# Kernel optimization log

Measured on AMD Instinct MI355X. Metric: run time of the kernel, lower is better.

Reference implementation:

```python
import jax, jax.numpy as jnp
import numpy as np

B, C, H, W = 4, 256, 128, 128
K = 3
BN = max(16, C // 4)  # 64
PAD = K // 2
EPS = 1e-5


def conv2d(x, w, b=None, pad=0):
    out = jax.lax.conv_general_dilated(
        x, w, (1, 1), [(pad, pad), (pad, pad)],
        dimension_numbers=("NCHW", "OIHW", "NCHW"))
    if b is not None:
        out = out + b[None, :, None, None]
    return out


def deform_conv2d(z, offset, mask, w, b):
    # torchvision modulated deform conv v2: offset [B,2*K*K,H,W] interleaved (dy,dx),
    # mask [B,K*K,H,W], kernel positions row-major, stride 1, pad PAD.
    Bz, Cb, Hz, Wz = z.shape
    K2 = K * K
    off = offset.reshape(Bz, K2, 2, Hz, Wz)
    ky, kx = jnp.meshgrid(jnp.arange(K), jnp.arange(K), indexing="ij")
    # sampling positions py/px: [B, K2, H, W]
    py = off[:, :, 0] + jnp.arange(Hz)[None, None, :, None] + (ky.reshape(K2) - PAD)[None, :, None, None]
    px = off[:, :, 1] + jnp.arange(Wz)[None, None, None, :] + (kx.reshape(K2) - PAD)[None, :, None, None]
    y0 = jnp.floor(py)
    x0 = jnp.floor(px)
    wy1 = py - y0  # frac weights
    wx1 = px - x0
    z_flat = z.reshape(Bz, Cb, Hz * Wz)

    def gather(yy, xx, wgt):
        valid = (yy >= 0) & (yy < Hz) & (xx >= 0) & (xx < Wz)
        yc = jnp.clip(yy, 0, Hz - 1).astype(jnp.int32)
        xc = jnp.clip(xx, 0, Wz - 1).astype(jnp.int32)
        idx = (yc * Wz + xc).reshape(Bz, K2 * Hz * Wz)
        g = jnp.take_along_axis(z_flat, idx[:, None, :], axis=2)  # [B, Cb, K2*H*W]
        g = g.reshape(Bz, Cb, K2, Hz, Wz)
        return g * (wgt * valid.astype(z.dtype))[:, None]

    val = (gather(y0, x0, (1 - wy1) * (1 - wx1))
           + gather(y0, x0 + 1, (1 - wy1) * wx1)
           + gather(y0 + 1, x0, wy1 * (1 - wx1))
           + gather(y0 + 1, x0 + 1, wy1 * wx1))
    val = val * mask[:, None]  # modulate: [B, Cb, K2, H, W]
    out = jnp.einsum("bckhw,ock->bohw", val, w.reshape(w.shape[0], Cb, K2))
    return out + b[None, :, None, None]


def setup_inputs() -> dict:
    key = jax.random.key(0)
    ks = jax.random.split(key, 11)
    s = 0.05
    return {
        "x": jax.random.normal(ks[0], (B, C, H, W), jnp.float32),
        "down_w": jax.random.normal(ks[1], (BN, C, 1, 1), jnp.float32) * s,
        "off_w": jax.random.normal(ks[2], (2 * K * K, BN, 3, 3), jnp.float32) * s,
        "off_b": jax.random.normal(ks[3], (2 * K * K,), jnp.float32) * s,
        "mask_w": jax.random.normal(ks[4], (K * K, BN, 3, 3), jnp.float32) * s,
        "mask_b": jax.random.normal(ks[5], (K * K,), jnp.float32) * s,
        "def_w": jax.random.normal(ks[6], (BN, BN, K, K), jnp.float32) * s,
        "def_b": jax.random.normal(ks[7], (BN,), jnp.float32) * s,
        "up_w": jax.random.normal(ks[8], (C, BN, 1, 1), jnp.float32) * s,
        "gamma": jnp.ones((C,), jnp.float32),
        "beta": jnp.zeros((C,), jnp.float32),
    }


def reference(x, down_w, off_w, off_b, mask_w, mask_b, def_w, def_b, up_w, gamma, beta):
    z = conv2d(x, down_w)                               # 1x1 down: [B, BN, H, W]
    offset = conv2d(z, off_w, off_b, pad=1)             # [B, 18, H, W]
    mask = jax.nn.sigmoid(conv2d(z, mask_w, mask_b, pad=1))  # [B, 9, H, W]
    z = deform_conv2d(z, offset, mask, def_w, def_b)    # [B, BN, H, W]
    z = conv2d(z, up_w)                                 # 1x1 up: [B, C, H, W]
    y = x + z
    # BatchNorm2d in training mode: batch statistics over (B, H, W), biased var
    mean = jnp.mean(y, axis=(0, 2, 3), keepdims=True)
    var = jnp.var(y, axis=(0, 2, 3), keepdims=True)
    yh = (y - mean) * jax.lax.rsqrt(var + EPS)
    yh = yh * gamma[None, :, None, None] + beta[None, :, None, None]
    return yh * jax.nn.sigmoid(yh)  # SiLU
```

## Files before the change

kernel.cpp:

```cpp
#include <hip/hip_runtime.h>
#include <hip/hip_bf16.h>


typedef __attribute__((ext_vector_type(8))) short bf16x8;
typedef __attribute__((ext_vector_type(4))) short bf16x4;
typedef __attribute__((ext_vector_type(4))) float f32x4;

#define HW   16384
#define CC   256
#define BNC  64

#define WS_STATS   0
#define WS_SS      131072
#define WS_FD      135168
#define WS_FOM     167936
#define WS_FDEF    204800
#define WS_FUP     278528
#define WS_ZBF     311296
#define WS_OM      8699904
#define WS_Z2      15777792

__device__ __forceinline__ short f2b(float f) {
    unsigned u = __float_as_uint(f);
    unsigned r = (u + 0x7FFFu + ((u >> 16) & 1u)) >> 16;
    return (short)r;
}
__device__ __forceinline__ float b2f(short s) {
    return __uint_as_float(((unsigned)(unsigned short)s) << 16);
}

__global__ void k_prep(const float* __restrict__ down_w, const float* __restrict__ off_w,
                       const float* __restrict__ mask_w, const float* __restrict__ def_w,
                       const float* __restrict__ up_w, char* __restrict__ ws) {
    int g = blockIdx.x * 256 + threadIdx.x;
    int row = g >> 6, lane = g & 63;
    if (row >= 172) return;
    int l15 = lane & 15, q = lane >> 4;
    short vals[8];
    short* dst;
    if (row < 32) {
        int nt = row >> 3, kk = row & 7;
        int n = nt * 16 + l15;
        for (int j = 0; j < 8; ++j) {
            int c = kk * 32 + q * 8 + j;
            vals[j] = f2b(down_w[n * 256 + c]);
        }
        dst = (short*)(ws + WS_FD) + row * 512 + lane * 8;
    } else if (row < 68) {
        int r = row - 32; int nt = r / 18, kk = r % 18;
        int n = nt * 16 + l15;
        for (int j = 0; j < 8; ++j) {
            int kap = kk * 32 + q * 8 + j; int k = kap >> 6, c = kap & 63;
            float v = 0.f;
            if (n < 18)      v = off_w[(n * 64 + c) * 9 + k];
            else if (n < 27) v = mask_w[((n - 18) * 64 + c) * 9 + k];
            vals[j] = f2b(v);
        }
        dst = (short*)(ws + WS_FOM) + r * 512 + lane * 8;
    } else if (row < 140) {
        int r = row - 68; int nt = r / 18, kk = r % 18;
        int n = nt * 16 + l15;
        int u = kk * 4 + q, k = u >> 3;
        for (int j = 0; j < 8; ++j) {
            int c = (u & 7) * 8 + j;
            vals[j] = f2b(def_w[(n * 64 + c) * 9 + k]);
        }
        dst = (short*)(ws + WS_FDEF) + r * 512 + lane * 8;
    } else {
        int r = row - 140; int nt = r >> 1, kk = r & 1;
        int o = nt * 16 + l15;
        for (int j = 0; j < 8; ++j) {
            int c = kk * 32 + q * 8 + j;
            vals[j] = f2b(up_w[o * 64 + c]);
        }
        dst = (short*)(ws + WS_FUP) + r * 512 + lane * 8;
    }
    for (int j = 0; j < 8; ++j) dst[j] = vals[j];
}

__global__ __launch_bounds__(256) void k_down(const float* __restrict__ x,
                                              const short* __restrict__ wfd,
                                              short* __restrict__ zbf) {
    __shared__ __align__(16) short xl[64 * 264];
    int blk = blockIdx.x;
    int b = blk >> 8;
    int hw0 = (blk & 255) * 64;
    int t = threadIdx.x;
    const float* xb = x + (size_t)b * CC * HW + hw0;
    int px = t & 63, w = t >> 6;
    for (int h = 0; h < 8; ++h) {
        int c0 = h * 32 + w * 8;
        bf16x8 pk;
        #pragma unroll
        for (int j = 0; j < 8; ++j)
            pk[j] = f2b(xb[(size_t)(c0 + j) * HW + px]);
        *(bf16x8*)(&xl[px * 264 + c0]) = pk;
    }
    __syncthreads();
    int lane = t & 63, wv = t >> 6;
    int l15 = lane & 15, q = lane >> 4;
    bf16x8 A[8];
    const short* xrow = &xl[(wv * 16 + l15) * 264];
    for (int kk = 0; kk < 8; ++kk)
        A[kk] = *(const bf16x8*)(xrow + kk * 32 + q * 8);
    const bf16x8* Bp = (const bf16x8*)wfd;
    size_t obase = ((size_t)b * HW + hw0 + wv * 16) * 64;
    for (int nt = 0; nt < 4; ++nt) {
        f32x4 acc = {0.f, 0.f, 0.f, 0.f};
        for (int kk = 0; kk < 8; ++kk) {
            bf16x8 Bf = Bp[(nt * 8 + kk) * 64 + lane];
            acc = __builtin_amdgcn_mfma_f32_16x16x32_bf16(A[kk], Bf, acc, 0, 0, 0);
        }
        int n = nt * 16 + l15;
        for (int r = 0; r < 4; ++r) {
            int prow = q * 4 + r;
            zbf[obase + (size_t)prow * 64 + n] = f2b(acc[r]);
        }
    }
}

__global__ __launch_bounds__(256) void k_offmask(const short* __restrict__ zbf,
                                                 const short* __restrict__ wfom,
                                                 const float* __restrict__ off_b,
                                                 const float* __restrict__ mask_b,
                                                 float* __restrict__ om) {
    int blk = blockIdx.x;
    int b = blk >> 8;
    int hw0 = (blk & 255) * 64;
    int y = hw0 >> 7, x0 = hw0 & 127;
    int t = threadIdx.x, lane = t & 63, wv = t >> 6;
    int l15 = lane & 15, q = lane >> 4;
    int xx0 = x0 + wv * 16 + l15;
    const short* zb = zbf + (size_t)b * HW * 64;
    f32x4 acc0 = {0, 0, 0, 0}, acc1 = {0, 0, 0, 0};
    const bf16x8* Bp = (const bf16x8*)wfom;
    for (int kk = 0; kk < 18; ++kk) {
        int k = kk >> 1;
        int yy = y + (k / 3) - 1;
        int xx = xx0 + (k % 3) - 1;
        int c0 = (kk & 1) * 32 + q * 8;
        bf16x8 A = {0, 0, 0, 0, 0, 0, 0, 0};
        if (yy >= 0 && yy < 128 && xx >= 0 && xx < 128)
            A = *(const bf16x8*)(zb + ((size_t)(yy * 128 + xx)) * 64 + c0);
        bf16x8 B0 = Bp[kk * 64 + lane];
        bf16x8 B1 = Bp[(18 + kk) * 64 + lane];
        acc0 = __builtin_amdgcn_mfma_f32_16x16x32_bf16(A, B0, acc0, 0, 0, 0);
        acc1 = __builtin_amdgcn_mfma_f32_16x16x32_bf16(A, B1, acc1, 0, 0, 0);
    }
    float* omb = om + ((size_t)b * HW + hw0 + wv * 16) * 27;
    for (int half = 0; half < 2; ++half) {
        f32x4 acc = half ? acc1 : acc0;
        int n = half * 16 + l15;
        if (n < 27) {
            for (int r = 0; r < 4; ++r) {
                int prow = q * 4 + r;
                float v = acc[r];
                if (n < 18) v += off_b[n];
                else { v += mask_b[n - 18]; v = 1.f / (1.f + __expf(-v)); }
                omb[prow * 27 + n] = v;
            }
        }
    }
}

__global__ __launch_bounds__(256) void k_deform(const short* __restrict__ zbf,
                                                const float* __restrict__ om,
                                                const short* __restrict__ wfdef,
                                                const float* __restrict__ def_b,
                                                short* __restrict__ z2) {
    __shared__ int4   pAi4[144];
    __shared__ float4 pAw4[144];
    __shared__ __align__(16) short valA[18 * 64 * 8];
    int blk = blockIdx.x;
    int b = blk >> 10;
    int hw0 = (blk & 1023) * 16;
    int y = hw0 >> 7, x0 = hw0 & 127;
    int t = threadIdx.x;
    if (t < 144) {
        int px = t / 9, k = t % 9;
        const float* p = om + ((size_t)b * HW + hw0 + px) * 27;
        float dy = p[2 * k], dx = p[2 * k + 1], m = p[18 + k];
        float py  = (float)y + (float)(k / 3 - 1) + dy;
        float pxf = (float)(x0 + px) + (float)(k % 3 - 1) + dx;
        float fy = floorf(py), fx = floorf(pxf);
        int iy = (int)fy, ix = (int)fx;
        float wy = py - fy, wx = pxf - fx;
        float ww[4] = { (1.f - wy) * (1.f - wx) * m, (1.f - wy) * wx * m,
                        wy * (1.f - wx) * m,          wy * wx * m };
        int ys[2] = {iy, iy + 1}, xs[2] = {ix, ix + 1};
        int   ri[4]; float rw[4];
        for (int ci = 0; ci < 4; ++ci) {
            int cy = ys[ci >> 1], cx = xs[ci & 1];
            bool v = (cy >= 0 && cy < 128 && cx >= 0 && cx < 128);
            ri[ci] = v ? (cy * 128 + cx) * 64 : 0;
            rw[ci] = v ? ww[ci] : 0.f;
        }
        pAi4[t] = make_int4(ri[0], ri[1], ri[2], ri[3]);
        pAw4[t] = make_float4(rw[0], rw[1], rw[2], rw[3]);
    }
    __syncthreads();
    const unsigned short* zb = (const unsigned short*)zbf + (size_t)b * HW * 64;
    for (int s = t; s < 1152; s += 256) {
        int px = s & 15, u = s >> 4;
        int k = u >> 3, cg = u & 7;
        int task = px * 9 + k;
        int4   idx = pAi4[task];
        float4 wt  = pAw4[task];
        int   ii[4] = { idx.x, idx.y, idx.z, idx.w };
        float wwt[4] = { wt.x, wt.y, wt.z, wt.w };
        float acc[8] = {0.f, 0.f, 0.f, 0.f, 0.f, 0.f, 0.f, 0.f};
        #pragma unroll
        for (int ci = 0; ci < 4; ++ci) {
            float w = wwt[ci];
            int4 d = *(const int4*)(zb + ii[ci] + cg * 8);
            int dp[4] = { d.x, d.y, d.z, d.w };
            #pragma unroll
            for (int p = 0; p < 4; ++p) {
                float lo = __uint_as_float((unsigned)dp[p] << 16);
                float hi = __uint_as_float((unsigned)dp[p] & 0xffff0000u);
                acc[2 * p]     += w * lo;
                acc[2 * p + 1] += w * hi;
            }
        }
        bf16x8 out;
        #pragma unroll
        for (int j = 0; j < 8; ++j) out[j] = f2b(acc[j]);
        *(bf16x8*)(&valA[s * 8]) = out;
    }
    __syncthreads();
    int lane = t & 63, wv = t >> 6;
    int l15 = lane & 15, q = lane >> 4;
    f32x4 acc = {0, 0, 0, 0};
    const bf16x8* Bp = (const bf16x8*)wfdef;
    const bf16x8* Ap = (const bf16x8*)valA;
    for (int kk = 0; kk < 18; ++kk) {
        bf16x8 A  = Ap[kk * 64 + lane];
        bf16x8 Bf = Bp[(wv * 18 + kk) * 64 + lane];
        acc = __builtin_amdgcn_mfma_f32_16x16x32_bf16(A, Bf, acc, 0, 0, 0);
    }
    int n = wv * 16 + l15;
    float bias = def_b[n];
    short* z2b = z2 + ((size_t)b * HW + hw0) * 64;
    for (int r = 0; r < 4; ++r) {
        int prow = q * 4 + r;
        z2b[prow * 64 + n] = f2b(acc[r] + bias);
    }
}

__global__ __launch_bounds__(256) void k_up(const short* __restrict__ z2,
                                            const short* __restrict__ wfup,
                                            const float* __restrict__ x,
                                            float* __restrict__ yout,
                                            float* __restrict__ stats) {
    __shared__ __align__(16) short yl[256 * 70];
    int blk = blockIdx.x;
    int b = blk >> 8;
    int hw0 = (blk & 255) * 64;
    int t = threadIdx.x, lane = t & 63, wv = t >> 6;
    int l15 = lane & 15, q = lane >> 4;
    const short* z2b = z2 + ((size_t)b * HW + hw0 + wv * 16) * 64;
    bf16x8 A0 = *(const bf16x8*)(z2b + (size_t)l15 * 64 + q * 8);
    bf16x8 A1 = *(const bf16x8*)(z2b + (size_t)l15 * 64 + 32 + q * 8);
    const bf16x8* Bp = (const bf16x8*)wfup;
    for (int nt = 0; nt < 16; ++nt) {
        f32x4 acc = {0, 0, 0, 0};
        acc = __builtin_amdgcn_mfma_f32_16x16x32_bf16(A0, Bp[(nt * 2 + 0) * 64 + lane], acc, 0, 0, 0);
        acc = __builtin_amdgcn_mfma_f32_16x16x32_bf16(A1, Bp[(nt * 2 + 1) * 64 + lane], acc, 0, 0, 0);
        int o = nt * 16 + l15;
        bf16x4 pk;
        #pragma unroll
        for (int r = 0; r < 4; ++r) pk[r] = f2b(acc[r]);
        *(bf16x4*)(&yl[o * 70 + wv * 16 + q * 4]) = pk;
    }
    __syncthreads();
    int i16 = t & 15, og = t >> 4;
    int bucket = blk & 63;
    size_t base = (size_t)b * CC * HW + hw0 + (size_t)i16 * 4;
    #pragma unroll
    for (int i = 0; i < 16; ++i) {
        int o = og + 16 * i;
        size_t pb = base + (size_t)o * HW;
        float4 xv = *(const float4*)(x + pb);
        bf16x4 uv = *(const bf16x4*)(&yl[o * 70 + i16 * 4]);
        float v0 = b2f(uv[0]) + xv.x;
        float v1 = b2f(uv[1]) + xv.y;
        float v2 = b2f(uv[2]) + xv.z;
        float v3 = b2f(uv[3]) + xv.w;
        *(float4*)(yout + pb) = make_float4(v0, v1, v2, v3);
        float s  = v0 + v1 + v2 + v3;
        float s2 = v0 * v0 + v1 * v1 + v2 * v2 + v3 * v3;
        #pragma unroll
        for (int m = 8; m >= 1; m >>= 1) { s += __shfl_xor(s, m); s2 += __shfl_xor(s2, m); }
        if (i16 == 0) {
            atomicAdd(&stats[bucket * 512 + o], s);
            atomicAdd(&stats[bucket * 512 + 256 + o], s2);
        }
    }
}

__global__ void k_stats(const float* __restrict__ stats, const float* __restrict__ gamma,
                        const float* __restrict__ beta, float* __restrict__ ss) {
    int o = threadIdx.x;
    float s = 0.f, s2 = 0.f;
    for (int u = 0; u < 64; ++u) { s += stats[u * 512 + o]; s2 += stats[u * 512 + 256 + o]; }
    float mean = s * (1.f / 65536.f);
    float var  = s2 * (1.f / 65536.f) - mean * mean;
    float rs = rsqrtf(var + 1e-5f);
    float sc = gamma[o] * rs;
    ss[o]       = sc;
    ss[256 + o] = beta[o] - mean * sc;
}

__global__ __launch_bounds__(256) void k_bn(float* __restrict__ y, const float* __restrict__ ss) {
    int g = blockIdx.x * 256 + threadIdx.x;
    int o = (g >> 10) & 255;
    float sc = ss[o], sh = ss[256 + o];
    float4* p = (float4*)y + (size_t)g * 4;
    for (int i = 0; i < 4; ++i) {
        float4 v = p[i];
        float vf[4] = { v.x, v.y, v.z, v.w };
        for (int j = 0; j < 4; ++j) {
            float h = vf[j] * sc + sh;
            vf[j] = h / (1.f + __expf(-h));
        }
        p[i] = make_float4(vf[0], vf[1], vf[2], vf[3]);
    }
}

extern "C" void kernel_launch(void* const* d_in, const int* in_sizes, int n_in,
                              void* d_out, int out_size, void* d_ws, size_t ws_size,
                              hipStream_t stream) {
    const float* x      = (const float*)d_in[0];
    const float* down_w = (const float*)d_in[1];
    const float* off_w  = (const float*)d_in[2];
    const float* off_b  = (const float*)d_in[3];
    const float* mask_w = (const float*)d_in[4];
    const float* mask_b = (const float*)d_in[5];
    const float* def_w  = (const float*)d_in[6];
    const float* def_b  = (const float*)d_in[7];
    const float* up_w   = (const float*)d_in[8];
    const float* gamma  = (const float*)d_in[9];
    const float* beta   = (const float*)d_in[10];
    char* ws = (char*)d_ws;
    float* stats = (float*)(ws + WS_STATS);
    float* ss    = (float*)(ws + WS_SS);
    short* wfd   = (short*)(ws + WS_FD);
    short* wfom  = (short*)(ws + WS_FOM);
    short* wfdef = (short*)(ws + WS_FDEF);
    short* wfup  = (short*)(ws + WS_FUP);
    short* zbf   = (short*)(ws + WS_ZBF);
    float* om    = (float*)(ws + WS_OM);
    short* z2    = (short*)(ws + WS_Z2);
    float* y     = (float*)d_out;

    hipMemsetAsync(stats, 0, 64 * 512 * sizeof(float), stream);
    hipLaunchKernelGGL(k_prep,    dim3(43),   dim3(256), 0, stream, down_w, off_w, mask_w, def_w, up_w, ws);
    hipLaunchKernelGGL(k_down,    dim3(1024), dim3(256), 0, stream, x, wfd, zbf);
    hipLaunchKernelGGL(k_offmask, dim3(1024), dim3(256), 0, stream, zbf, wfom, off_b, mask_b, om);
    hipLaunchKernelGGL(k_deform,  dim3(4096), dim3(256), 0, stream, zbf, om, wfdef, def_b, z2);
    hipLaunchKernelGGL(k_up,      dim3(1024), dim3(256), 0, stream, z2, wfup, x, y, stats);
    hipLaunchKernelGGL(k_stats,   dim3(1),    dim3(256), 0, stream, stats, gamma, beta, ss);
    hipLaunchKernelGGL(k_bn,      dim3(4096), dim3(256), 0, stream, y, ss);
}
```

Before: 251.2 us.

## Tile deform conv as 4x4 pixel blocks with LDS-staged neighbourhood of z

Each deform block now covers a 4x4 spatial tile instead of a 16-pixel row strip. Before sampling, it stages a clamped 13x13 pixel halo of the bf16 z tensor into LDS, using a rotated channel-group swizzle to avoid bank conflicts. Bilinear taps that fall entirely inside the halo read from LDS, and the rest fall back to global loads. This trades an up-front 21KB LDS load per block, which is more pixels than the tile needs and may lower occupancy, for fewer scattered global gathers.

Result: no change. 246.5 us (-1.9%).

```diff
diff --git a/kernel.cpp b/kernel.cpp
--- a/kernel.cpp
+++ b/kernel.cpp
@@ -168,64 +168,96 @@
                                                 const short* __restrict__ wfdef,
                                                 const float* __restrict__ def_b,
                                                 short* __restrict__ z2) {
+    __shared__ __align__(16) short ldsZ[169 * 64];
     __shared__ int4   pAi4[144];
     __shared__ float4 pAw4[144];
+    __shared__ int    pAf[144];
     __shared__ __align__(16) short valA[18 * 64 * 8];
     int blk = blockIdx.x;
     int b = blk >> 10;
-    int hw0 = (blk & 1023) * 16;
-    int y = hw0 >> 7, x0 = hw0 & 127;
+    int tile = blk & 1023;
+    int yt = (tile >> 5) << 2, xt = (tile & 31) << 2;
+    int sy0 = yt - 4; sy0 = sy0 < 0 ? 0 : (sy0 > 115 ? 115 : sy0);
+    int sx0 = xt - 4; sx0 = sx0 < 0 ? 0 : (sx0 > 115 ? 115 : sx0);
     int t = threadIdx.x;
+    const short* zbs = zbf + (size_t)b * HW * 64;
+    for (int u = t; u < 1352; u += 256) {
+        int r = u / 104, rem = u - r * 104;
+        int p = rem >> 3, cg = rem & 7;
+        int gp = (sy0 + r) * 128 + sx0 + p;
+        int lpix = r * 13 + p;
+        int slot = (cg + lpix) & 7;
+        *(int4*)(&ldsZ[lpix * 64 + slot * 8]) = *(const int4*)(zbs + (size_t)gp * 64 + cg * 8);
+    }
     if (t < 144) {
         int px = t / 9, k = t % 9;
-        const float* p = om + ((size_t)b * HW + hw0 + px) * 27;
+        int oy = yt + (px >> 2), ox = xt + (px & 3);
+        const float* p = om + ((size_t)b * HW + oy * 128 + ox) * 27;
         float dy = p[2 * k], dx = p[2 * k + 1], m = p[18 + k];
-        float py  = (float)y + (float)(k / 3 - 1) + dy;
-        float pxf = (float)(x0 + px) + (float)(k % 3 - 1) + dx;
+        float py  = (float)oy + (float)(k / 3 - 1) + dy;
+        float pxf = (float)ox + (float)(k % 3 - 1) + dx;
         float fy = floorf(py), fx = floorf(pxf);
         int iy = (int)fy, ix = (int)fx;
         float wy = py - fy, wx = pxf - fx;
         float ww[4] = { (1.f - wy) * (1.f - wx) * m, (1.f - wy) * wx * m,
                         wy * (1.f - wx) * m,          wy * wx * m };
+        bool flg = (iy >= sy0) && (iy + 1 <= sy0 + 12) && (ix >= sx0) && (ix + 1 <= sx0 + 12);
         int ys[2] = {iy, iy + 1}, xs[2] = {ix, ix + 1};
         int   ri[4]; float rw[4];
         for (int ci = 0; ci < 4; ++ci) {
             int cy = ys[ci >> 1], cx = xs[ci & 1];
-            bool v = (cy >= 0 && cy < 128 && cx >= 0 && cx < 128);
-            ri[ci] = v ? (cy * 128 + cx) * 64 : 0;
-            rw[ci] = v ? ww[ci] : 0.f;
+            if (flg) {
+                int lp = (cy - sy0) * 13 + (cx - sx0);
+                ri[ci] = (lp << 6) | (lp & 7);
+                rw[ci] = ww[ci];
+            } else {
+                bool v = (cy >= 0 && cy < 128 && cx >= 0 && cx < 128);
+                ri[ci] = v ? (cy * 128 + cx) * 64 : 0;
+                rw[ci] = v ? ww[ci] : 0.f;
+            }
         }
         pAi4[t] = make_int4(ri[0], ri[1], ri[2], ri[3]);
         pAw4[t] = make_float4(rw[0], rw[1], rw[2], rw[3]);
+        pAf[t]  = flg ? 1 : 0;
     }
     __syncthreads();
-    const unsigned short* zb = (const unsigned short*)zbf + (size_t)b * HW * 64;
-    for (int s = t; s < 1152; s += 256) {
-        int px = s & 15, u = s >> 4;
-        int k = u >> 3, cg = u & 7;
-        int task = px * 9 + k;
-        int4   idx = pAi4[task];
-        float4 wt  = pAw4[task];
-        int   ii[4] = { idx.x, idx.y, idx.z, idx.w };
-        float wwt[4] = { wt.x, wt.y, wt.z, wt.w };
-        float acc[8] = {0.f, 0.f, 0.f, 0.f, 0.f, 0.f, 0.f, 0.f};
-        #pragma unroll
-        for (int ci = 0; ci < 4; ++ci) {
-            float w = wwt[ci];
-            int4 d = *(const int4*)(zb + ii[ci] + cg * 8);
-            int dp[4] = { d.x, d.y, d.z, d.w };
+    for (int it = 0; it < 5; ++it) {
+        int s = t + it * 256;
+        if (s < 1152) {
+            int px = s & 15, u = s >> 4;
+            int k = u >> 3, cg = u & 7;
+            int task = px * 9 + k;
+            int4   idx = pAi4[task];
+            float4 wt  = pAw4[task];
+            int    flg = pAf[task];
+            int   ii[4] = { idx.x, idx.y, idx.z, idx.w };
+            float wwt[4] = { wt.x, wt.y, wt.z, wt.w };
+            int cgs = cg * 8;
+            float acc[8] = {0.f, 0.f, 0.f, 0.f, 0.f, 0.f, 0.f, 0.f};
             #pragma unroll
-            for (int p = 0; p < 4; ++p) {
-                float lo = __uint_as_float((unsigned)dp[p] << 16);
-                float hi = __uint_as_float((unsigned)dp[p] & 0xffff0000u);
-                acc[2 * p]     += w * lo;
-                acc[2 * p + 1] += w * hi;
+            for (int ci = 0; ci < 4; ++ci) {
+                float w = wwt[ci];
+                int4 d;
+                if (flg) {
+                    int v = ii[ci];
+                    d = *(const int4*)(&ldsZ[(v & ~63) + (((cg + (v & 7)) & 7) << 3)]);
+                } else {
+                    d = *(const int4*)(zbs + ii[ci] + cgs);
+                }
+                int dp[4] = { d.x, d.y, d.z, d.w };
+                #pragma unroll
+                for (int p = 0; p < 4; ++p) {
+                    float lo = __uint_as_float((unsigned)dp[p] << 16);
+                    float hi = __uint_as_float((unsigned)dp[p] & 0xffff0000u);
+                    acc[2 * p]     += w * lo;
+                    acc[2 * p + 1] += w * hi;
+                }
             }
-        }
-        bf16x8 out;
-        #pragma unroll
-        for (int j = 0; j < 8; ++j) out[j] = f2b(acc[j]);
-        *(bf16x8*)(&valA[s * 8]) = out;
+            bf16x8 out;
+            #pragma unroll
+            for (int j = 0; j < 8; ++j) out[j] = f2b(acc[j]);
+            *(bf16x8*)(&valA[s * 8]) = out;
+        }
     }
     __syncthreads();
     int lane = t & 63, wv = t >> 6;
@@ -240,10 +272,11 @@
     }
     int n = wv * 16 + l15;
     float bias = def_b[n];
-    short* z2b = z2 + ((size_t)b * HW + hw0) * 64;
+    short* z2b = z2 + (size_t)b * HW * 64;
     for (int r = 0; r < 4; ++r) {
         int prow = q * 4 + r;
-        z2b[prow * 64 + n] = f2b(acc[r] + bias);
+        int hw = (yt + (prow >> 2)) * 128 + xt + (prow & 3);
+        z2b[(size_t)hw * 64 + n] = f2b(acc[r] + bias);
     }
 }
 
```
